# Kernel tuning notes

Hardware: AMD Instinct MI355X
Metric: run time of the kernel (lower is better)

## Reference

```python
import jax, jax.numpy as jnp
import numpy as np

N = 100000          # total nodes in batch of junction trees
H = 256             # hidden_size
K = 8               # MAX_NUM_NEIGHBORS (padded neighbor slots)


def setup_inputs() -> dict:
    key = jax.random.key(0)
    k1, k2, k3, k4, k5, k6, k7 = jax.random.split(key, 7)
    scale = 1.0 / np.sqrt(H)
    inputs = {
        "prev_layer_output": jax.random.normal(k1, (N, H), dtype=jnp.float32),
        "W_U": jax.random.uniform(k2, (H, H), jnp.float32, -scale, scale),
        "W_V": jax.random.uniform(k3, (H, H), jnp.float32, -scale, scale),
        "W_A": jax.random.uniform(k4, (H, H), jnp.float32, -scale, scale),
        "W_B": jax.random.uniform(k5, (H, H), jnp.float32, -scale, scale),
        "parent_idxs": jnp.arange(N, dtype=jnp.int32),
        "child_idxs": jax.random.randint(k6, (N, K), 0, N, dtype=jnp.int32),
        "child_mask": jax.random.randint(k7, (N, K), 0, 2, dtype=jnp.int32).astype(jnp.bool_),
    }
    return inputs


def reference(prev_layer_output, W_U, W_V, W_A, W_B, parent_idxs, child_idxs, child_mask):
    # Gather parent hidden states: [E, H]
    ph = prev_layer_output[parent_idxs]
    # Gather child hidden states, zeroing padded slots (faithful to the
    # zero-vector padding in the original): [E, K, H]
    ch = jnp.where(child_mask[..., None], prev_layer_output[child_idxs], 0.0)

    # Edge gates: eta = sigmoid(A(parent)[:,None] + B(child)).
    # Padded slots still contribute sigmoid(A(parent)) — matches original.
    A_h = jnp.einsum('eh,ih->ei', ph, W_A)            # [E, H]
    B_h = jnp.einsum('ekh,ih->eki', ch, W_B)          # [E, K, H]
    eta = jax.nn.sigmoid(A_h[:, None, :] + B_h)       # [E, K, H]

    # Graph convolution: relu(U(parent) + sum_k (eta + V(child)))
    # NOTE: original ADDS eta to V_h (despite the 'mul' variable name).
    U_h = jnp.einsum('eh,ih->ei', ph, W_U)            # [E, H]
    V_h = jnp.einsum('ekh,ih->eki', ch, W_V)          # [E, K, H]
    new_h = jax.nn.relu(U_h + jnp.sum(eta + V_h, axis=1))  # [E, H]

    # Scatter into the current layer output (rows not updated stay zero).
    current = jnp.zeros_like(prev_layer_output).at[parent_idxs].set(new_h)
    return current
```

## Files before the change

kernel.cpp:

```cpp
#include <hip/hip_runtime.h>

#define HH 256
#define KK 8

typedef __attribute__((ext_vector_type(8))) short s16x8;
typedef __attribute__((ext_vector_type(4))) float f32x4;
typedef __attribute__((address_space(3))) unsigned int lds_u32;
typedef const __attribute__((address_space(1))) unsigned int glb_u32;

__device__ __forceinline__ float bf2f(unsigned short u){ unsigned x=((unsigned)u)<<16; return __builtin_bit_cast(float,x); }
__device__ __forceinline__ unsigned short f2bf(float f){ unsigned x=__builtin_bit_cast(unsigned,f); return (unsigned short)((x+0x7fffu+((x>>16)&1u))>>16); }
__device__ __forceinline__ float sigmoidf(float x){ return __builtin_amdgcn_rcpf(1.0f + __expf(-x)); }

__global__ void cvt_w(const float* __restrict__ wa, const float* __restrict__ wu,
                      const float* __restrict__ wv, const float* __restrict__ wbm,
                      unsigned short* __restrict__ dst){
  const int w = blockIdx.y;
  const float* src = (w==0)? wa : (w==1)? wu : (w==2)? wv : wbm;
  const int i = blockIdx.x*256 + threadIdx.x;
  const float4* s = reinterpret_cast<const float4*>(src);
  float4 a = s[i*2], b = s[i*2+1];
  uint4 o;
  o.x = (unsigned)f2bf(a.x) | ((unsigned)f2bf(a.y)<<16);
  o.y = (unsigned)f2bf(a.z) | ((unsigned)f2bf(a.w)<<16);
  o.z = (unsigned)f2bf(b.x) | ((unsigned)f2bf(b.y)<<16);
  o.w = (unsigned)f2bf(b.z) | ((unsigned)f2bf(b.w)<<16);
  reinterpret_cast<uint4*>(dst + (size_t)w*65536)[i] = o;
}

__global__ __launch_bounds__(512, 4)
void gemm_all(const float* __restrict__ prev,
              const unsigned short* __restrict__ wb,
              unsigned short* __restrict__ px,
              int n)
{
  __shared__ char smem[65536];
  const int tid = threadIdx.x;
  const int m0  = blockIdx.x * 128;
  const int lane = tid & 63, wid = tid >> 6;
  const int wr = wid >> 1, wc = wid & 1;
  const int lm = lane & 15, kc = lane >> 4;

  #pragma unroll
  for (int it=0; it<8; ++it){
    const int c = it*512 + tid;
    const int row = c>>5, kch = c&31;
    const int gm = m0 + row;
    uint4 o = {0u,0u,0u,0u};
    if (gm < n){
      const float4* sp = reinterpret_cast<const float4*>(prev + (size_t)gm*HH + kch*8);
      float4 f0 = sp[0], f1 = sp[1];
      o.x=(unsigned)f2bf(f0.x)|((unsigned)f2bf(f0.y)<<16);
      o.y=(unsigned)f2bf(f0.z)|((unsigned)f2bf(f0.w)<<16);
      o.z=(unsigned)f2bf(f1.x)|((unsigned)f2bf(f1.y)<<16);
      o.w=(unsigned)f2bf(f1.z)|((unsigned)f2bf(f1.w)<<16);
    }
    *reinterpret_cast<uint4*>(smem + row*512 + ((kch*16) ^ ((row&7)<<4))) = o;
  }
  __syncthreads();

  s16x8 af[2][8];
  #pragma unroll
  for (int i=0;i<2;++i){
    const int row = wr*32 + i*16 + lm;
    #pragma unroll
    for (int k8=0;k8<8;++k8)
      af[i][k8] = *reinterpret_cast<const s16x8*>(smem + row*512 + ((k8*64 + kc*16) ^ ((row&7)<<4)));
  }
  __syncthreads();

  const int rr = lane>>4, ks16 = (lane&15)*16;
  const int off_e = rr*512 + (ks16 ^ (rr<<4));
  const char* wbc = reinterpret_cast<const char*>(wb);

  #define ISSUE_PANEL(Wp, lb)                                                      \
    { _Pragma("unroll")                                                            \
      for (int c_=0;c_<4;++c_){                                                    \
        const int chunk_ = wid*4 + c_;                                             \
        const char* ga_ = (Wp) + chunk_*2048 + ((c_&1)? (off_e^64) : off_e);       \
        __builtin_amdgcn_global_load_lds((glb_u32*)ga_,                            \
            (lds_u32*)((lb) + chunk_*1024), 16, 0, 0);                             \
      } }

  ISSUE_PANEL(wbc, smem)

  f32x4 acc[2][4];
  for (int g=0; g<8; ++g){
    #pragma unroll
    for (int kh=0; kh<2; ++kh){
      __syncthreads();
      if (kh==0){
        ISSUE_PANEL(wbc + g*65536 + 256, smem + 32768)
      } else if (g < 7){
        ISSUE_PANEL(wbc + (g+1)*65536, smem)
      }
      if (kh==0){
        #pragma unroll
        for (int i=0;i<2;++i)
          #pragma unroll
          for (int j=0;j<4;++j) acc[i][j]=(f32x4){0.f,0.f,0.f,0.f};
      }
      const char* rb = smem + kh*32768;
      #pragma unroll
      for (int kk=0; kk<4; ++kk){
        #pragma unroll
        for (int j=0;j<4;++j){
          const int brow = wc*64 + j*16 + lm;
          s16x8 bf = *reinterpret_cast<const s16x8*>(rb + brow*256 + ((kk*64 + kc*16) ^ ((brow&7)<<4)));
          acc[0][j] = __builtin_amdgcn_mfma_f32_16x16x32_bf16(af[0][kh*4+kk], bf, acc[0][j], 0, 0, 0);
          acc[1][j] = __builtin_amdgcn_mfma_f32_16x16x32_bf16(af[1][kh*4+kk], bf, acc[1][j], 0, 0, 0);
        }
      }
      if (kh==1){
        #pragma unroll
        for (int i=0;i<2;++i){
          #pragma unroll
          for (int r=0;r<4;++r){
            const int gm = m0 + wr*32 + i*16 + kc*4 + r;
            if (gm < n){
              unsigned short* dp = px + (size_t)gm*1024 + g*128 + wc*64 + lm;
              #pragma unroll
              for (int j=0;j<4;++j) dp[j*16] = f2bf(acc[i][j][r]);
            }
          }
        }
      }
    }
  }
  #undef ISSUE_PANEL
}

__global__ __launch_bounds__(256)
void epilogue(const unsigned short* __restrict__ px,
              const int* __restrict__ parent,
              const int* __restrict__ child,
              const int* __restrict__ mask,
              float* __restrict__ out,
              int n)
{
  const int e = blockIdx.x*8 + (threadIdx.x>>5);
  if (e >= n) return;
  const int c8 = (threadIdx.x & 31) * 8;
  const int p  = parent[e];

  const unsigned short* rp = px + (size_t)p*1024 + c8;
  uint4 av = *reinterpret_cast<const uint4*>(rp);
  uint4 uv = *reinterpret_cast<const uint4*>(rp + 256);
  const unsigned short* ap = reinterpret_cast<const unsigned short*>(&av);
  const unsigned short* up = reinterpret_cast<const unsigned short*>(&uv);

  float A[8], o[8], eta[8];
  #pragma unroll
  for (int j=0;j<8;++j){ A[j]=bf2f(ap[j]); o[j]=bf2f(up[j]); eta[j]=0.f; }

  int nm = 0;
  #pragma unroll
  for (int k=0;k<KK;++k){
    if (mask[(size_t)e*KK + k]){
      const unsigned short* rc = px + (size_t)child[(size_t)e*KK + k]*1024 + c8;
      uint4 pv = *reinterpret_cast<const uint4*>(rc + 512);
      uint4 pb = *reinterpret_cast<const uint4*>(rc + 768);
      const unsigned short* vp = reinterpret_cast<const unsigned short*>(&pv);
      const unsigned short* bp = reinterpret_cast<const unsigned short*>(&pb);
      #pragma unroll
      for (int j=0;j<8;++j){
        o[j]   += bf2f(vp[j]);
        eta[j] += sigmoidf(A[j] + bf2f(bp[j]));
      }
    } else ++nm;
  }

  const float fnm = (float)nm;
  #pragma unroll
  for (int j=0;j<8;++j){
    float s = o[j] + eta[j] + fnm * sigmoidf(A[j]);
    out[(size_t)p*HH + c8 + j] = s > 0.f ? s : 0.f;
  }
}

extern "C" void kernel_launch(void* const* d_in, const int* in_sizes, int n_in,
                              void* d_out, int out_size, void* d_ws, size_t ws_size,
                              hipStream_t stream)
{
  const float* prev = (const float*)d_in[0];
  const float* W_U  = (const float*)d_in[1];
  const float* W_V  = (const float*)d_in[2];
  const float* W_A  = (const float*)d_in[3];
  const float* W_B  = (const float*)d_in[4];
  const int* parent = (const int*)d_in[5];
  const int* child  = (const int*)d_in[6];
  const int* mask   = (const int*)d_in[7];
  float* out = (float*)d_out;

  const int n_nodes = in_sizes[5];

  unsigned short* wb = (unsigned short*)d_ws;
  unsigned short* px = wb + 4*65536;

  dim3 gc(32, 4);
  cvt_w<<<gc, 256, 0, stream>>>(W_A, W_U, W_V, W_B, wb);

  gemm_all<<<(n_nodes + 127)/128, 512, 0, stream>>>(prev, wb, px, n_nodes);

  epilogue<<<(n_nodes + 7)/8, 256, 0, stream>>>(px, parent, child, mask, out, n_nodes);
}
```

Measured before the change: 225.1 us.

## Deepen weight-panel pipeline to four smaller LDS stages with explicit vmcnt waits

The GEMM's weight staging changes from two 32 KB half-panels, each guarded by a full __syncthreads, to four 16 KB stages (64 output columns by 128 K each) issued three stages ahead. Each wait uses an explicit s_waitcnt vmcnt plus s_barrier instead of draining all outstanding loads. MFMA sections are raised with s_setprio, and the per-wave accumulator tile shrinks from 2x4 to 2x2, which frees registers. The aim is to hide global-to-LDS weight latency behind compute, at the cost of more barriers (32 iterations instead of 16) and more, smaller output stores.

```diff
diff --git a/kernel.cpp b/kernel.cpp
--- a/kernel.cpp
+++ b/kernel.cpp
@@ -75,53 +75,56 @@
 
   #define ISSUE_PANEL(Wp, lb)                                                      \
     { _Pragma("unroll")                                                            \
-      for (int c_=0;c_<4;++c_){                                                    \
-        const int chunk_ = wid*4 + c_;                                             \
-        const char* ga_ = (Wp) + chunk_*2048 + ((c_&1)? (off_e^64) : off_e);       \
+      for (int c_=0;c_<2;++c_){                                                    \
+        const int chunk_ = wid*2 + c_;                                             \
+        const char* ga_ = (Wp) + chunk_*2048 + ((chunk_&1)? (off_e^64) : off_e);   \
         __builtin_amdgcn_global_load_lds((glb_u32*)ga_,                            \
             (lds_u32*)((lb) + chunk_*1024), 16, 0, 0);                             \
       } }
 
-  ISSUE_PANEL(wbc, smem)
-
-  f32x4 acc[2][4];
-  for (int g=0; g<8; ++g){
+  ISSUE_PANEL(wbc,         smem)
+  ISSUE_PANEL(wbc + 256,   smem + 16384)
+  ISSUE_PANEL(wbc + 32768, smem + 32768)
+
+  f32x4 acc[2][2];
+  for (int q=0; q<32; ++q){
+    if (q < 30)       asm volatile("s_waitcnt vmcnt(4)" ::: "memory");
+    else if (q == 30) asm volatile("s_waitcnt vmcnt(2)" ::: "memory");
+    else              asm volatile("s_waitcnt vmcnt(0)" ::: "memory");
+    __builtin_amdgcn_s_barrier();
+    __builtin_amdgcn_sched_barrier(0);
+    if (q < 29){
+      const int p3 = q + 3;
+      ISSUE_PANEL(wbc + (p3>>1)*32768 + (p3&1)*256, smem + (p3&3)*16384)
+    }
+    const int g = q>>1, kh = q&1;
+    const char* rb = smem + (q&3)*16384;
+    if (kh==0){
+      acc[0][0]=(f32x4){0.f,0.f,0.f,0.f}; acc[0][1]=(f32x4){0.f,0.f,0.f,0.f};
+      acc[1][0]=(f32x4){0.f,0.f,0.f,0.f}; acc[1][1]=(f32x4){0.f,0.f,0.f,0.f};
+    }
+    __builtin_amdgcn_s_setprio(1);
     #pragma unroll
-    for (int kh=0; kh<2; ++kh){
-      __syncthreads();
-      if (kh==0){
-        ISSUE_PANEL(wbc + g*65536 + 256, smem + 32768)
-      } else if (g < 7){
-        ISSUE_PANEL(wbc + (g+1)*65536, smem)
+    for (int kk=0; kk<4; ++kk){
+      #pragma unroll
+      for (int j=0;j<2;++j){
+        const int brow = wc*32 + j*16 + lm;
+        s16x8 bf = *reinterpret_cast<const s16x8*>(rb + brow*256 + ((kk*64 + kc*16) ^ ((brow&7)<<4)));
+        acc[0][j] = __builtin_amdgcn_mfma_f32_16x16x32_bf16(af[0][kh*4+kk], bf, acc[0][j], 0, 0, 0);
+        acc[1][j] = __builtin_amdgcn_mfma_f32_16x16x32_bf16(af[1][kh*4+kk], bf, acc[1][j], 0, 0, 0);
       }
-      if (kh==0){
+    }
+    __builtin_amdgcn_s_setprio(0);
+    if (kh==1){
+      #pragma unroll
+      for (int i=0;i<2;++i){
         #pragma unroll
-        for (int i=0;i<2;++i)
-          #pragma unroll
-          for (int j=0;j<4;++j) acc[i][j]=(f32x4){0.f,0.f,0.f,0.f};
-      }
-      const char* rb = smem + kh*32768;
-      #pragma unroll
-      for (int kk=0; kk<4; ++kk){
-        #pragma unroll
-        for (int j=0;j<4;++j){
-          const int brow = wc*64 + j*16 + lm;
-          s16x8 bf = *reinterpret_cast<const s16x8*>(rb + brow*256 + ((kk*64 + kc*16) ^ ((brow&7)<<4)));
-          acc[0][j] = __builtin_amdgcn_mfma_f32_16x16x32_bf16(af[0][kh*4+kk], bf, acc[0][j], 0, 0, 0);
-          acc[1][j] = __builtin_amdgcn_mfma_f32_16x16x32_bf16(af[1][kh*4+kk], bf, acc[1][j], 0, 0, 0);
-        }
-      }
-      if (kh==1){
-        #pragma unroll
-        for (int i=0;i<2;++i){
-          #pragma unroll
-          for (int r=0;r<4;++r){
-            const int gm = m0 + wr*32 + i*16 + kc*4 + r;
-            if (gm < n){
-              unsigned short* dp = px + (size_t)gm*1024 + g*128 + wc*64 + lm;
-              #pragma unroll
-              for (int j=0;j<4;++j) dp[j*16] = f2bf(acc[i][j][r]);
-            }
+        for (int r=0;r<4;++r){
+          const int gm = m0 + wr*32 + i*16 + kc*4 + r;
+          if (gm < n){
+            unsigned short* dp = px + (size_t)gm*1024 + g*64 + wc*32 + lm;
+            dp[0]  = f2bf(acc[i][0][r]);
+            dp[16] = f2bf(acc[i][1][r]);
           }
         }
       }
```

New measurement: 448.8 us. 99.4% more time.

## Replace LDS-staged GEMM with register-only GEMM reading weights from global/L2

Applied to the files above, without the earlier changes.

Each wave now loads its 32 activation rows directly from global into registers, converting them to bf16, and streams all 1024 weight columns straight from global memory (expected to hit L2) instead of staging weight panels in LDS with async loads and barriers. This removes shared memory use and block-wide synchronisation, and allows more resident waves. In exchange, every wave rereads the full 512KB bf16 weight set from cache, the B loads are no longer shared across waves, and the 2-byte scattered stores to px stay narrow.

```diff
diff --git a/kernel.cpp b/kernel.cpp
--- a/kernel.cpp
+++ b/kernel.cpp
@@ -5,8 +5,6 @@
 
 typedef __attribute__((ext_vector_type(8))) short s16x8;
 typedef __attribute__((ext_vector_type(4))) float f32x4;
-typedef __attribute__((address_space(3))) unsigned int lds_u32;
-typedef const __attribute__((address_space(1))) unsigned int glb_u32;
 
 __device__ __forceinline__ float bf2f(unsigned short u){ unsigned x=((unsigned)u)<<16; return __builtin_bit_cast(float,x); }
 __device__ __forceinline__ unsigned short f2bf(float f){ unsigned x=__builtin_bit_cast(unsigned,f); return (unsigned short)((x+0x7fffu+((x>>16)&1u))>>16); }
@@ -28,106 +26,60 @@
   reinterpret_cast<uint4*>(dst + (size_t)w*65536)[i] = o;
 }
 
-__global__ __launch_bounds__(512, 4)
-void gemm_all(const float* __restrict__ prev,
+__global__ __launch_bounds__(256, 4)
+void gemm_reg(const float* __restrict__ prev,
               const unsigned short* __restrict__ wb,
               unsigned short* __restrict__ px,
               int n)
 {
-  __shared__ char smem[65536];
-  const int tid = threadIdx.x;
-  const int m0  = blockIdx.x * 128;
+  const int tid  = threadIdx.x;
   const int lane = tid & 63, wid = tid >> 6;
-  const int wr = wid >> 1, wc = wid & 1;
-  const int lm = lane & 15, kc = lane >> 4;
-
-  #pragma unroll
-  for (int it=0; it<8; ++it){
-    const int c = it*512 + tid;
-    const int row = c>>5, kch = c&31;
-    const int gm = m0 + row;
-    uint4 o = {0u,0u,0u,0u};
-    if (gm < n){
-      const float4* sp = reinterpret_cast<const float4*>(prev + (size_t)gm*HH + kch*8);
-      float4 f0 = sp[0], f1 = sp[1];
-      o.x=(unsigned)f2bf(f0.x)|((unsigned)f2bf(f0.y)<<16);
-      o.y=(unsigned)f2bf(f0.z)|((unsigned)f2bf(f0.w)<<16);
-      o.z=(unsigned)f2bf(f1.x)|((unsigned)f2bf(f1.y)<<16);
-      o.w=(unsigned)f2bf(f1.z)|((unsigned)f2bf(f1.w)<<16);
-    }
-    *reinterpret_cast<uint4*>(smem + row*512 + ((kch*16) ^ ((row&7)<<4))) = o;
-  }
-  __syncthreads();
+  const int r0   = blockIdx.x * 128 + wid * 32;
+  const int lm   = lane & 15, kc = lane >> 4;
 
   s16x8 af[2][8];
   #pragma unroll
   for (int i=0;i<2;++i){
-    const int row = wr*32 + i*16 + lm;
-    #pragma unroll
-    for (int k8=0;k8<8;++k8)
-      af[i][k8] = *reinterpret_cast<const s16x8*>(smem + row*512 + ((k8*64 + kc*16) ^ ((row&7)<<4)));
-  }
-  __syncthreads();
-
-  const int rr = lane>>4, ks16 = (lane&15)*16;
-  const int off_e = rr*512 + (ks16 ^ (rr<<4));
-  const char* wbc = reinterpret_cast<const char*>(wb);
-
-  #define ISSUE_PANEL(Wp, lb)                                                      \
-    { _Pragma("unroll")                                                            \
-      for (int c_=0;c_<4;++c_){                                                    \
-        const int chunk_ = wid*4 + c_;                                             \
-        const char* ga_ = (Wp) + chunk_*2048 + ((c_&1)? (off_e^64) : off_e);       \
-        __builtin_amdgcn_global_load_lds((glb_u32*)ga_,                            \
-            (lds_u32*)((lb) + chunk_*1024), 16, 0, 0);                             \
-      } }
-
-  ISSUE_PANEL(wbc, smem)
-
-  f32x4 acc[2][4];
-  for (int g=0; g<8; ++g){
-    #pragma unroll
-    for (int kh=0; kh<2; ++kh){
-      __syncthreads();
-      if (kh==0){
-        ISSUE_PANEL(wbc + g*65536 + 256, smem + 32768)
-      } else if (g < 7){
-        ISSUE_PANEL(wbc + (g+1)*65536, smem)
+    const int row = r0 + i*16 + lm;
+    if (row < n){
+      const char* rp = reinterpret_cast<const char*>(prev + (size_t)row * HH);
+      #pragma unroll
+      for (int kk=0;kk<8;++kk){
+        float4 f0 = *reinterpret_cast<const float4*>(rp + kk*128 + kc*32);
+        float4 f1 = *reinterpret_cast<const float4*>(rp + kk*128 + kc*32 + 16);
+        s16x8 a;
+        a[0]=(short)f2bf(f0.x); a[1]=(short)f2bf(f0.y);
+        a[2]=(short)f2bf(f0.z); a[3]=(short)f2bf(f0.w);
+        a[4]=(short)f2bf(f1.x); a[5]=(short)f2bf(f1.y);
+        a[6]=(short)f2bf(f1.z); a[7]=(short)f2bf(f1.w);
+        af[i][kk] = a;
       }
-      if (kh==0){
-        #pragma unroll
-        for (int i=0;i<2;++i)
-          #pragma unroll
-          for (int j=0;j<4;++j) acc[i][j]=(f32x4){0.f,0.f,0.f,0.f};
-      }
-      const char* rb = smem + kh*32768;
+    } else {
       #pragma unroll
-      for (int kk=0; kk<4; ++kk){
-        #pragma unroll
-        for (int j=0;j<4;++j){
-          const int brow = wc*64 + j*16 + lm;
-          s16x8 bf = *reinterpret_cast<const s16x8*>(rb + brow*256 + ((kk*64 + kc*16) ^ ((brow&7)<<4)));
-          acc[0][j] = __builtin_amdgcn_mfma_f32_16x16x32_bf16(af[0][kh*4+kk], bf, acc[0][j], 0, 0, 0);
-          acc[1][j] = __builtin_amdgcn_mfma_f32_16x16x32_bf16(af[1][kh*4+kk], bf, acc[1][j], 0, 0, 0);
-        }
-      }
-      if (kh==1){
-        #pragma unroll
-        for (int i=0;i<2;++i){
-          #pragma unroll
-          for (int r=0;r<4;++r){
-            const int gm = m0 + wr*32 + i*16 + kc*4 + r;
-            if (gm < n){
-              unsigned short* dp = px + (size_t)gm*1024 + g*128 + wc*64 + lm;
-              #pragma unroll
-              for (int j=0;j<4;++j) dp[j*16] = f2bf(acc[i][j][r]);
-            }
-          }
-        }
-      }
+      for (int kk=0;kk<8;++kk) af[i][kk] = (s16x8){0,0,0,0,0,0,0,0};
     }
   }
-  #undef ISSUE_PANEL
+
+  const char* wbc = reinterpret_cast<const char*>(wb);
+  for (int cg=0; cg<64; ++cg){
+    const char* bp = wbc + (size_t)(cg*16 + lm)*512 + kc*16;
+    f32x4 acc0 = {0.f,0.f,0.f,0.f}, acc1 = {0.f,0.f,0.f,0.f};
+    s16x8 b[8];
+    #pragma unroll
+    for (int kk=0;kk<8;++kk) b[kk] = *reinterpret_cast<const s16x8*>(bp + kk*64);
+    #pragma unroll
+    for (int kk=0;kk<8;++kk){
+      acc0 = __builtin_amdgcn_mfma_f32_16x16x32_bf16(af[0][kk], b[kk], acc0, 0, 0, 0);
+      acc1 = __builtin_amdgcn_mfma_f32_16x16x32_bf16(af[1][kk], b[kk], acc1, 0, 0, 0);
+    }
+    #pragma unroll
+    for (int r=0;r<4;++r){
+      const int row0 = r0 + kc*4 + r;
+      if (row0 < n)      px[(size_t)row0*1024 + cg*16 + lm]      = f2bf(acc0[r]);
+      const int row1 = row0 + 16;
+      if (row1 < n)      px[(size_t)row1*1024 + cg*16 + lm]      = f2bf(acc1[r]);
+    }
+  }
 }
 
 __global__ __launch_bounds__(256)
@@ -200,7 +152,7 @@
   dim3 gc(32, 4);
   cvt_w<<<gc, 256, 0, stream>>>(W_A, W_U, W_V, W_B, wb);
 
-  gemm_all<<<(n_nodes + 127)/128, 512, 0, stream>>>(prev, wb, px, n_nodes);
+  gemm_reg<<<(n_nodes + 127)/128, 256, 0, stream>>>(prev, wb, px, n_nodes);
 
   epilogue<<<(n_nodes + 7)/8, 256, 0, stream>>>(px, parent, child, mask, out, n_nodes);
 }
```

Result: slower. 365.5 us (+62.4%).
